# Optimization experiments

Hardware: AMD Instinct MI355X
Metric: run time of the kernel (lower is better)

Reference implementation:

```python
import jax, jax.numpy as jnp
import numpy as np

TEMPERATURE = 0.1
BASE_TEMPERATURE = 0.07
N = 8192
D = 128


def setup_inputs() -> dict:
    key = jax.random.key(0)
    kf, kl = jax.random.split(key)
    feats = jax.random.normal(kf, (N, 1, D), dtype=jnp.float32)
    # contrastive embeddings are typically L2-normalized upstream
    feats = feats / jnp.linalg.norm(feats, axis=-1, keepdims=True)
    labels = jax.random.randint(kl, (N,), 0, 2, dtype=jnp.int32)
    return {"feats": feats, "labels": labels}


def reference(feats, labels):
    # feats: [anchor_num, n_view=1, D]; labels: [anchor_num] binary fg/bg
    anchor_num, n_view, d = feats.shape
    n = anchor_num * n_view  # n_view == 1 in this module
    contrast_feature = feats.reshape(n, d)

    lab = labels.reshape(-1, 1)
    pos_mask = (lab == lab.T).astype(feats.dtype)  # [N, N]
    neg_mask = 1.0 - pos_mask

    # [N, N] similarity logits
    logits = jnp.matmul(contrast_feature, contrast_feature.T) / TEMPERATURE
    logits_max = jax.lax.stop_gradient(jnp.max(logits, axis=1, keepdims=True))
    logits = logits - logits_max

    # mask out self-contrast on the diagonal (logits_mask in torch code)
    idx = jnp.arange(n)
    pos_mask = pos_mask.at[idx, idx].set(0.0)

    exp_logits = jnp.exp(logits)
    neg_logits = jnp.sum(exp_logits * neg_mask, axis=1, keepdims=True)  # [N,1]
    log_prob = logits - jnp.log(exp_logits + neg_logits)

    mean_log_prob_pos = jnp.sum(pos_mask * log_prob, axis=1) / jnp.sum(pos_mask, axis=1)
    loss = -(TEMPERATURE / BASE_TEMPERATURE) * mean_log_prob_pos
    return jnp.mean(loss)
```

## Files before the change

kernel.cpp:

```cpp
#include <hip/hip_runtime.h>
#include <hip/hip_bf16.h>

#define NN 8192
#define DD 128

typedef short bf16x8 __attribute__((ext_vector_type(8)));
typedef float f32x4 __attribute__((ext_vector_type(4)));

#define LOG2E 1.4426950408889634f
#define K2f   14.426950408889634f

#define M_OFF    (NN * DD * 2)
#define LABF_OFF (M_OFF + NN * 4)
#define G_OFF    (LABF_OFF + NN * 4)
#define CNT_OFF  (G_OFF + 256 * 4)
#define EG_OFF   (CNT_OFF + 256)
#define ELG_OFF  (EG_OFF + NN * 4)

#define BROWS 256
#define BCOLS 512
#define TCOLS 32
#define ITERS (BCOLS / TCOLS)

__device__ __forceinline__ unsigned short f2bf(float x) {
    unsigned u = __float_as_uint(x);
    u = (u + 0x7FFFu + ((u >> 16) & 1u)) >> 16;
    return (unsigned short)u;
}

__global__ __launch_bounds__(256) void prep_kernel(const float* __restrict__ F,
        const int* __restrict__ labels, unsigned short* __restrict__ F16,
        float* __restrict__ M, float* __restrict__ labf, float* __restrict__ G,
        int* __restrict__ cnt1, float* __restrict__ Eg, float* __restrict__ Elg) {
    __shared__ float sG[256];
    __shared__ int scnt;
    const int tid = threadIdx.x;
    sG[tid] = 0.f;
    if (tid == 0) scnt = 0;
    __syncthreads();
    const int wave = tid >> 6, lane = tid & 63;
    const int half = lane >> 5, l32 = lane & 31;
    const int rb = blockIdx.x * 32;
    if (tid < 32) { Eg[rb + tid] = 0.f; Elg[rb + tid] = 0.f; }
    int mycnt = 0;
    float g1a[4] = {0.f, 0.f, 0.f, 0.f}, gta[4] = {0.f, 0.f, 0.f, 0.f};
    #pragma unroll
    for (int it = 0; it < 4; ++it) {
        const int row = rb + it * 8 + wave * 2 + half;
        const int lab = labels[row];
        const float lf = (float)lab;
        const float4 f = *reinterpret_cast<const float4*>(F + row * DD + l32 * 4);
        ushort4 u;
        u.x = f2bf(f.x); u.y = f2bf(f.y); u.z = f2bf(f.z); u.w = f2bf(f.w);
        *reinterpret_cast<ushort4*>(F16 + row * DD + l32 * 4) = u;
        g1a[0] = fmaf(lf, f.x, g1a[0]); gta[0] += f.x;
        g1a[1] = fmaf(lf, f.y, g1a[1]); gta[1] += f.y;
        g1a[2] = fmaf(lf, f.z, g1a[2]); gta[2] += f.z;
        g1a[3] = fmaf(lf, f.w, g1a[3]); gta[3] += f.w;
        float ss = fmaf(f.x, f.x, fmaf(f.y, f.y, fmaf(f.z, f.z, f.w * f.w)));
        #pragma unroll
        for (int off = 1; off < 32; off <<= 1) ss += __shfl_xor(ss, off);
        if (l32 == 0) {
            M[row] = 10.0f * ss;
            labf[row] = lf;
            mycnt += lab;
        }
    }
    #pragma unroll
    for (int j = 0; j < 4; ++j) {
        atomicAdd(&sG[l32 * 4 + j], g1a[j]);
        atomicAdd(&sG[128 + l32 * 4 + j], gta[j]);
    }
    if (l32 == 0 && mycnt) atomicAdd(&scnt, mycnt);
    __syncthreads();
    atomicAdd(&G[tid], sG[tid]);
    if (tid == 0) atomicAdd(cnt1, scnt);
}

__global__ __launch_bounds__(512, 4) void loss_kernel(
        const unsigned short* __restrict__ F16, const float* __restrict__ M,
        const float* __restrict__ labf, float* __restrict__ Eg,
        float* __restrict__ Elg) {
    __shared__ unsigned short Bt[2][TCOLS * DD];
    __shared__ float Lab[BCOLS];
    const int tid  = threadIdx.x;
    const int wave = tid >> 6, lane = tid & 63;
    const int quad = lane >> 4, l16 = lane & 15;
    const int rb = (blockIdx.x & 31) * BROWS;
    const int cb = (blockIdx.x >> 5) * BCOLS;

    Lab[tid] = labf[cb + tid];

    const int rw = rb + wave * 32;
    bf16x8 a[2][4];
    #pragma unroll
    for (int m = 0; m < 2; m++)
        #pragma unroll
        for (int kb = 0; kb < 4; kb++)
            a[m][kb] = *reinterpret_cast<const bf16x8*>(
                F16 + (rw + m * 16 + l16) * DD + kb * 32 + quad * 8);

    float mneg[2][4];
    #pragma unroll
    for (int m = 0; m < 2; m++)
        #pragma unroll
        for (int r = 0; r < 4; r++)
            mneg[m][r] = -M[rw + m * 16 + quad * 4 + r] * LOG2E;

    const int scol = tid >> 4;
    const int sc   = tid & 15;
    const unsigned short* sbase = F16 + (cb + scol) * DD + sc * 8;
    const int sdst = sc * (TCOLS * 8) + (((scol ^ sc) & 31) * 8);

    *reinterpret_cast<bf16x8*>(&Bt[0][sdst]) =
        *reinterpret_cast<const bf16x8*>(sbase);

    float accE[2][4] = {}, accEl[2][4] = {};
    __syncthreads();

    for (int it = 0; it < ITERS; ++it) {
        const int cur = it & 1;
        const int itn = (it + 1) & (ITERS - 1);
        const bf16x8 vn = *reinterpret_cast<const bf16x8*>(sbase + itn * TCOLS * DD);

        #pragma unroll
        for (int g = 0; g < 2; ++g) {
            bf16x8 bfr[4];
            #pragma unroll
            for (int kb = 0; kb < 4; kb++) {
                const int cr = kb * 4 + quad;
                const int col = g * 16 + l16;
                bfr[kb] = *reinterpret_cast<const bf16x8*>(
                    &Bt[cur][cr * (TCOLS * 8) + (((col ^ cr) & 31) * 8)]);
            }
            f32x4 d0 = {0.f, 0.f, 0.f, 0.f}, d1 = {0.f, 0.f, 0.f, 0.f};
            #pragma unroll
            for (int kb = 0; kb < 4; kb++) {
                d0 = __builtin_amdgcn_mfma_f32_16x16x32_bf16(a[0][kb], bfr[kb], d0, 0, 0, 0);
                d1 = __builtin_amdgcn_mfma_f32_16x16x32_bf16(a[1][kb], bfr[kb], d1, 0, 0, 0);
            }
            const float lc = Lab[it * TCOLS + g * 16 + l16];
            #pragma unroll
            for (int m = 0; m < 2; m++) {
                #pragma unroll
                for (int r = 0; r < 4; r++) {
                    const float vv = (m == 0) ? d0[r] : d1[r];
                    const float e = exp2f(fmaf(vv, K2f, mneg[m][r]));
                    accE[m][r] += e;
                    accEl[m][r] = fmaf(lc, e, accEl[m][r]);
                }
            }
        }

        *reinterpret_cast<bf16x8*>(&Bt[cur ^ 1][sdst]) = vn;
        __syncthreads();
    }

    #pragma unroll
    for (int m = 0; m < 2; m++) {
        #pragma unroll
        for (int r = 0; r < 4; r++) {
            float e = accE[m][r], el = accEl[m][r];
            #pragma unroll
            for (int off = 1; off < 16; off <<= 1) {
                e  += __shfl_xor(e,  off);
                el += __shfl_xor(el, off);
            }
            if (l16 == 0) {
                const int row = rw + m * 16 + quad * 4 + r;
                atomicAdd(&Eg[row], e);
                atomicAdd(&Elg[row], el);
            }
        }
    }
}

__global__ __launch_bounds__(256) void final_kernel(
        const unsigned short* __restrict__ F16, const float* __restrict__ M,
        const int* __restrict__ labels, const float* __restrict__ G,
        const int* __restrict__ cnt1, const float* __restrict__ Eg,
        const float* __restrict__ Elg, float* __restrict__ out) {
    __shared__ float sG[256];
    __shared__ float wsum[4];
    const int tid = threadIdx.x;
    sG[tid] = G[tid];
    __syncthreads();
    const int row = blockIdx.x * 256 + tid;
    const int lr = labels[row];
    float dot = 0.f;
    const unsigned short* f = F16 + row * DD;
    #pragma unroll
    for (int k = 0; k < DD; k += 8) {
        const bf16x8 fv = *reinterpret_cast<const bf16x8*>(f + k);
        #pragma unroll
        for (int j = 0; j < 8; j++) {
            const float fj = __uint_as_float(((unsigned)(unsigned short)fv[j]) << 16);
            const float g1 = sG[k + j];
            const float gl = lr ? g1 : (sG[128 + k + j] - g1);
            dot = fmaf(fj, gl, dot);
        }
    }
    const float E    = Eg[row];
    const float El   = Elg[row];
    const float Epos = lr ? El : (E - El);
    const float Si   = E - Epos;
    const float mi   = M[row];
    const int   c1   = *cnt1;
    const float cntp1 = (float)(lr ? c1 : (NN - c1));
    const float cnt   = cntp1 - 1.f;
    const float sum_l   = fmaf(10.f, dot, -cntp1 * mi);
    const float sum_log = cntp1 * __logf(Si) + Epos / Si;
    float li = -(10.f / 7.f) * (sum_l - sum_log) / cnt;
    #pragma unroll
    for (int off = 1; off < 64; off <<= 1) li += __shfl_xor(li, off);
    if ((tid & 63) == 0) wsum[tid >> 6] = li;
    __syncthreads();
    if (tid == 0)
        atomicAdd(out, (wsum[0] + wsum[1] + wsum[2] + wsum[3]) * (1.0f / NN));
}

extern "C" void kernel_launch(void* const* d_in, const int* in_sizes, int n_in,
                              void* d_out, int out_size, void* d_ws, size_t ws_size,
                              hipStream_t stream) {
    const float* F      = (const float*)d_in[0];
    const int*   labels = (const int*)d_in[1];
    float*       out    = (float*)d_out;
    char*        ws     = (char*)d_ws;
    unsigned short* F16 = (unsigned short*)ws;
    float*       M      = (float*)(ws + M_OFF);
    float*       labf   = (float*)(ws + LABF_OFF);
    float*       G      = (float*)(ws + G_OFF);
    int*         cnt1   = (int*)(ws + CNT_OFF);
    float*       Eg     = (float*)(ws + EG_OFF);
    float*       Elg    = (float*)(ws + ELG_OFF);

    hipMemsetAsync(out, 0, sizeof(float), stream);
    hipMemsetAsync(ws + G_OFF, 0, 256 * 4 + 256, stream);

    prep_kernel<<<NN / 32, 256, 0, stream>>>(F, labels, F16, M, labf, G, cnt1, Eg, Elg);
    loss_kernel<<<512, 512, 0, stream>>>(F16, M, labf, Eg, Elg);
    final_kernel<<<NN / 256, 256, 0, stream>>>(F16, M, labels, G, cnt1, Eg, Elg, out);
}
```

Before: 105.6 us.

## Fold logit scale into bf16 features, drop row max, widen per-wave row tile

Features are pre-scaled by sqrt(10*log2e) when converted to bf16, so the MFMA result feeds exp2 directly. The per-row max shift (M) is removed entirely, since it cancels algebraically in the log-softmax. This saves the norm reduction, the M buffer and an FMA per element. The loss kernel now runs 256-thread blocks in which each wave covers 64 rows (4 MFMA row tiles), so each B fragment read from LDS is reused twice as often, at the cost of more registers and fewer waves. Without the max shift, exp can overflow if feature norms are large; it is safe for unit-norm inputs.

```diff
diff --git a/kernel.cpp b/kernel.cpp
--- a/kernel.cpp
+++ b/kernel.cpp
@@ -7,11 +7,10 @@
 typedef short bf16x8 __attribute__((ext_vector_type(8)));
 typedef float f32x4 __attribute__((ext_vector_type(4)));
 
-#define LOG2E 1.4426950408889634f
-#define K2f   14.426950408889634f
-
-#define M_OFF    (NN * DD * 2)
-#define LABF_OFF (M_OFF + NN * 4)
+#define CSCALE  3.7982829f
+#define SLSCALE 2.6327684f
+
+#define LABF_OFF (NN * DD * 2)
 #define G_OFF    (LABF_OFF + NN * 4)
 #define CNT_OFF  (G_OFF + 256 * 4)
 #define EG_OFF   (CNT_OFF + 256)
@@ -30,7 +29,7 @@
 
 __global__ __launch_bounds__(256) void prep_kernel(const float* __restrict__ F,
         const int* __restrict__ labels, unsigned short* __restrict__ F16,
-        float* __restrict__ M, float* __restrict__ labf, float* __restrict__ G,
+        float* __restrict__ labf, float* __restrict__ G,
         int* __restrict__ cnt1, float* __restrict__ Eg, float* __restrict__ Elg) {
     __shared__ float sG[256];
     __shared__ int scnt;
@@ -51,17 +50,14 @@
         const float lf = (float)lab;
         const float4 f = *reinterpret_cast<const float4*>(F + row * DD + l32 * 4);
         ushort4 u;
-        u.x = f2bf(f.x); u.y = f2bf(f.y); u.z = f2bf(f.z); u.w = f2bf(f.w);
+        u.x = f2bf(CSCALE * f.x); u.y = f2bf(CSCALE * f.y);
+        u.z = f2bf(CSCALE * f.z); u.w = f2bf(CSCALE * f.w);
         *reinterpret_cast<ushort4*>(F16 + row * DD + l32 * 4) = u;
         g1a[0] = fmaf(lf, f.x, g1a[0]); gta[0] += f.x;
         g1a[1] = fmaf(lf, f.y, g1a[1]); gta[1] += f.y;
         g1a[2] = fmaf(lf, f.z, g1a[2]); gta[2] += f.z;
         g1a[3] = fmaf(lf, f.w, g1a[3]); gta[3] += f.w;
-        float ss = fmaf(f.x, f.x, fmaf(f.y, f.y, fmaf(f.z, f.z, f.w * f.w)));
-        #pragma unroll
-        for (int off = 1; off < 32; off <<= 1) ss += __shfl_xor(ss, off);
         if (l32 == 0) {
-            M[row] = 10.0f * ss;
             labf[row] = lf;
             mycnt += lab;
         }
@@ -77,10 +73,9 @@
     if (tid == 0) atomicAdd(cnt1, scnt);
 }
 
-__global__ __launch_bounds__(512, 4) void loss_kernel(
-        const unsigned short* __restrict__ F16, const float* __restrict__ M,
-        const float* __restrict__ labf, float* __restrict__ Eg,
-        float* __restrict__ Elg) {
+__global__ __launch_bounds__(256, 2) void loss_kernel(
+        const unsigned short* __restrict__ F16, const float* __restrict__ labf,
+        float* __restrict__ Eg, float* __restrict__ Elg) {
     __shared__ unsigned short Bt[2][TCOLS * DD];
     __shared__ float Lab[BCOLS];
     const int tid  = threadIdx.x;
@@ -89,39 +84,37 @@
     const int rb = (blockIdx.x & 31) * BROWS;
     const int cb = (blockIdx.x >> 5) * BCOLS;
 
-    Lab[tid] = labf[cb + tid];
-
-    const int rw = rb + wave * 32;
-    bf16x8 a[2][4];
-    #pragma unroll
-    for (int m = 0; m < 2; m++)
+    Lab[tid]       = labf[cb + tid];
+    Lab[tid + 256] = labf[cb + tid + 256];
+
+    const int rw = rb + wave * 64;
+    bf16x8 a[4][4];
+    #pragma unroll
+    for (int m = 0; m < 4; m++)
         #pragma unroll
         for (int kb = 0; kb < 4; kb++)
             a[m][kb] = *reinterpret_cast<const bf16x8*>(
                 F16 + (rw + m * 16 + l16) * DD + kb * 32 + quad * 8);
 
-    float mneg[2][4];
-    #pragma unroll
-    for (int m = 0; m < 2; m++)
-        #pragma unroll
-        for (int r = 0; r < 4; r++)
-            mneg[m][r] = -M[rw + m * 16 + quad * 4 + r] * LOG2E;
-
-    const int scol = tid >> 4;
-    const int sc   = tid & 15;
-    const unsigned short* sbase = F16 + (cb + scol) * DD + sc * 8;
-    const int sdst = sc * (TCOLS * 8) + (((scol ^ sc) & 31) * 8);
-
-    *reinterpret_cast<bf16x8*>(&Bt[0][sdst]) =
+    const int scol = tid >> 3;
+    const int sc0  = (tid & 7) * 2;
+    const unsigned short* sbase = F16 + (cb + scol) * DD + sc0 * 8;
+    const int sdst0 = sc0 * (TCOLS * 8) + (((scol ^ sc0) & 31) * 8);
+    const int sdst1 = (sc0 + 1) * (TCOLS * 8) + (((scol ^ (sc0 + 1)) & 31) * 8);
+
+    *reinterpret_cast<bf16x8*>(&Bt[0][sdst0]) =
         *reinterpret_cast<const bf16x8*>(sbase);
-
-    float accE[2][4] = {}, accEl[2][4] = {};
+    *reinterpret_cast<bf16x8*>(&Bt[0][sdst1]) =
+        *reinterpret_cast<const bf16x8*>(sbase + 8);
+
+    float accE[4][4] = {}, accEl[4][4] = {};
     __syncthreads();
 
     for (int it = 0; it < ITERS; ++it) {
         const int cur = it & 1;
         const int itn = (it + 1) & (ITERS - 1);
-        const bf16x8 vn = *reinterpret_cast<const bf16x8*>(sbase + itn * TCOLS * DD);
+        const bf16x8 vn0 = *reinterpret_cast<const bf16x8*>(sbase + itn * TCOLS * DD);
+        const bf16x8 vn1 = *reinterpret_cast<const bf16x8*>(sbase + itn * TCOLS * DD + 8);
 
         #pragma unroll
         for (int g = 0; g < 2; ++g) {
@@ -134,30 +127,35 @@
                     &Bt[cur][cr * (TCOLS * 8) + (((col ^ cr) & 31) * 8)]);
             }
             f32x4 d0 = {0.f, 0.f, 0.f, 0.f}, d1 = {0.f, 0.f, 0.f, 0.f};
+            f32x4 d2 = {0.f, 0.f, 0.f, 0.f}, d3 = {0.f, 0.f, 0.f, 0.f};
             #pragma unroll
             for (int kb = 0; kb < 4; kb++) {
                 d0 = __builtin_amdgcn_mfma_f32_16x16x32_bf16(a[0][kb], bfr[kb], d0, 0, 0, 0);
                 d1 = __builtin_amdgcn_mfma_f32_16x16x32_bf16(a[1][kb], bfr[kb], d1, 0, 0, 0);
+                d2 = __builtin_amdgcn_mfma_f32_16x16x32_bf16(a[2][kb], bfr[kb], d2, 0, 0, 0);
+                d3 = __builtin_amdgcn_mfma_f32_16x16x32_bf16(a[3][kb], bfr[kb], d3, 0, 0, 0);
             }
             const float lc = Lab[it * TCOLS + g * 16 + l16];
             #pragma unroll
-            for (int m = 0; m < 2; m++) {
-                #pragma unroll
-                for (int r = 0; r < 4; r++) {
-                    const float vv = (m == 0) ? d0[r] : d1[r];
-                    const float e = exp2f(fmaf(vv, K2f, mneg[m][r]));
-                    accE[m][r] += e;
-                    accEl[m][r] = fmaf(lc, e, accEl[m][r]);
-                }
-            }
-        }
-
-        *reinterpret_cast<bf16x8*>(&Bt[cur ^ 1][sdst]) = vn;
+            for (int r = 0; r < 4; r++) {
+                const float e0 = exp2f(d0[r]);
+                accE[0][r] += e0; accEl[0][r] = fmaf(lc, e0, accEl[0][r]);
+                const float e1 = exp2f(d1[r]);
+                accE[1][r] += e1; accEl[1][r] = fmaf(lc, e1, accEl[1][r]);
+                const float e2 = exp2f(d2[r]);
+                accE[2][r] += e2; accEl[2][r] = fmaf(lc, e2, accEl[2][r]);
+                const float e3 = exp2f(d3[r]);
+                accE[3][r] += e3; accEl[3][r] = fmaf(lc, e3, accEl[3][r]);
+            }
+        }
+
+        *reinterpret_cast<bf16x8*>(&Bt[cur ^ 1][sdst0]) = vn0;
+        *reinterpret_cast<bf16x8*>(&Bt[cur ^ 1][sdst1]) = vn1;
         __syncthreads();
     }
 
     #pragma unroll
-    for (int m = 0; m < 2; m++) {
+    for (int m = 0; m < 4; m++) {
         #pragma unroll
         for (int r = 0; r < 4; r++) {
             float e = accE[m][r], el = accEl[m][r];
@@ -176,7 +174,7 @@
 }
 
 __global__ __launch_bounds__(256) void final_kernel(
-        const unsigned short* __restrict__ F16, const float* __restrict__ M,
+        const unsigned short* __restrict__ F16,
         const int* __restrict__ labels, const float* __restrict__ G,
         const int* __restrict__ cnt1, const float* __restrict__ Eg,
         const float* __restrict__ Elg, float* __restrict__ out) {
@@ -204,11 +202,10 @@
     const float El   = Elg[row];
     const float Epos = lr ? El : (E - El);
     const float Si   = E - Epos;
-    const float mi   = M[row];
     const int   c1   = *cnt1;
     const float cntp1 = (float)(lr ? c1 : (NN - c1));
     const float cnt   = cntp1 - 1.f;
-    const float sum_l   = fmaf(10.f, dot, -cntp1 * mi);
+    const float sum_l   = SLSCALE * dot;
     const float sum_log = cntp1 * __logf(Si) + Epos / Si;
     float li = -(10.f / 7.f) * (sum_l - sum_log) / cnt;
     #pragma unroll
@@ -227,7 +224,6 @@
     float*       out    = (float*)d_out;
     char*        ws     = (char*)d_ws;
     unsigned short* F16 = (unsigned short*)ws;
-    float*       M      = (float*)(ws + M_OFF);
     float*       labf   = (float*)(ws + LABF_OFF);
     float*       G      = (float*)(ws + G_OFF);
     int*         cnt1   = (int*)(ws + CNT_OFF);
@@ -237,7 +233,7 @@
     hipMemsetAsync(out, 0, sizeof(float), stream);
     hipMemsetAsync(ws + G_OFF, 0, 256 * 4 + 256, stream);
 
-    prep_kernel<<<NN / 32, 256, 0, stream>>>(F, labels, F16, M, labf, G, cnt1, Eg, Elg);
-    loss_kernel<<<512, 512, 0, stream>>>(F16, M, labf, Eg, Elg);
-    final_kernel<<<NN / 256, 256, 0, stream>>>(F16, M, labels, G, cnt1, Eg, Elg, out);
-}
+    prep_kernel<<<NN / 32, 256, 0, stream>>>(F, labels, F16, labf, G, cnt1, Eg, Elg);
+    loss_kernel<<<512, 256, 0, stream>>>(F16, labf, Eg, Elg);
+    final_kernel<<<NN / 256, 256, 0, stream>>>(F16, labels, G, cnt1, Eg, Elg, out);
+}
```

New measurement: 107.7 us. 2.1% more time.
